# Performance work log

Hardware: AMD Instinct MI355X
Metric: run time of the kernel (lower is better)

## Reference

```python
import jax, jax.numpy as jnp
import numpy as np

N_NODES = 50000
N_EDGES = 800000
F_IN = 4
PERIODS = 8
H_DIM = 32


def setup_inputs() -> dict:
    key = jax.random.key(0)
    ks = jax.random.split(key, 20)
    s = lambda *sh: 1.0 / np.sqrt(sh[0])
    inp = {
        "x": jax.random.normal(ks[0], (N_NODES, F_IN, PERIODS), jnp.float32),
        "edge_index": jax.random.randint(ks[1], (2, N_EDGES), 0, N_NODES, jnp.int32),
        # GCNConv weights/biases for z, r, h gates (glorot-ish init)
        "Wz": jax.random.normal(ks[2], (F_IN, H_DIM), jnp.float32) * s(F_IN),
        "bz": jnp.zeros((H_DIM,), jnp.float32),
        "Wr": jax.random.normal(ks[3], (F_IN, H_DIM), jnp.float32) * s(F_IN),
        "br": jnp.zeros((H_DIM,), jnp.float32),
        "Wh": jax.random.normal(ks[4], (F_IN, H_DIM), jnp.float32) * s(F_IN),
        "bh": jnp.zeros((H_DIM,), jnp.float32),
        # torch.nn.Linear(2*H, H) for each gate; stored as [2H, H] for x @ W
        "LzW": jax.random.normal(ks[5], (2 * H_DIM, H_DIM), jnp.float32) * s(2 * H_DIM),
        "Lzb": jnp.zeros((H_DIM,), jnp.float32),
        "LrW": jax.random.normal(ks[6], (2 * H_DIM, H_DIM), jnp.float32) * s(2 * H_DIM),
        "Lrb": jnp.zeros((H_DIM,), jnp.float32),
        "LhW": jax.random.normal(ks[7], (2 * H_DIM, H_DIM), jnp.float32) * s(2 * H_DIM),
        "Lhb": jnp.zeros((H_DIM,), jnp.float32),
        # A3TGCN attention over periods (uniform init in PyG-T)
        "att": jax.random.uniform(ks[8], (PERIODS,), jnp.float32),
        # final Linear(32, periods)
        "outW": jax.random.normal(ks[9], (H_DIM, PERIODS), jnp.float32) * s(H_DIM),
        "outb": jnp.zeros((PERIODS,), jnp.float32),
    }
    return inp


def _forward(x, edge_index, Wz, bz, Wr, br, Wh, bh, LzW, Lzb, LrW, Lrb, LhW, Lhb, att, outW, outb):
    N = x.shape[0]
    src, dst = edge_index[0], edge_index[1]
    # GCN symmetric normalization with added self loops (edge_weight = 1)
    deg = jax.ops.segment_sum(jnp.ones(src.shape[0], x.dtype), dst, num_segments=N) + 1.0
    dinv = jnp.where(deg > 0, deg ** -0.5, 0.0)
    enorm = dinv[src] * dinv[dst]          # [E]
    snorm = dinv * dinv                    # self-loop norm, [N]

    def gcn(xt, W, b):
        h = xt @ W                                             # [N, 32]
        agg = jax.ops.segment_sum(enorm[:, None] * h[src], dst, num_segments=N)
        return agg + snorm[:, None] * h + b

    H0 = jnp.zeros((N, H_DIM), x.dtype)  # A3TGCN passes H=None each period
    probs = jax.nn.softmax(att)

    def step(acc, inputs):
        xt, p = inputs                                          # xt: [N, F]
        Z = jax.nn.sigmoid(jnp.concatenate([gcn(xt, Wz, bz), H0], axis=1) @ LzW + Lzb)
        R = jax.nn.sigmoid(jnp.concatenate([gcn(xt, Wr, br), H0], axis=1) @ LrW + Lrb)
        Ht = jnp.tanh(jnp.concatenate([gcn(xt, Wh, bh), H0 * R], axis=1) @ LhW + Lhb)
        H = Z * H0 + (1.0 - Z) * Ht
        return acc + p * H, None

    xs = jnp.moveaxis(x, 2, 0)             # [P, N, F]
    H_accum, _ = jax.lax.scan(step, jnp.zeros((N, H_DIM), x.dtype), (xs, probs))
    return jax.nn.relu(H_accum) @ outW + outb  # [N, periods]


def reference(x, edge_index, Wz, bz, Wr, br, Wh, bh, LzW, Lzb, LrW, Lrb, LhW, Lhb, att, outW, outb):
    return _forward(x, edge_index, Wz, bz, Wr, br, Wh, bh, LzW, Lzb, LrW, Lrb, LhW, Lhb, att, outW, outb)
```

## Files before the change

kernel.cpp:

```cpp
#include <hip/hip_runtime.h>


#define NN 50000
#define NE 800000
#define SLAB 48
#define NG 8
#define NPG (NN / NG)
#define FBLK 4096
#define GPB (FBLK / NG)
#define PBASE 0xAAAAAAAAu

#define OFF_CNT 0
#define OFF_PP  50048
#define OFF_CSR 50688

__device__ __forceinline__ int realdeg(int v) {
    unsigned dp = (unsigned)v - PBASE;
    return (dp < (1u << 20)) ? (int)dp : v;
}

__global__ __launch_bounds__(256) void k_fill(const int* ei, int* cnt,
        unsigned short* csr,
        const float* Wz, const float* bz, const float* Wh, const float* bh,
        const float* LzW, const float* Lzb, const float* LhW, const float* Lhb,
        const float* att, const float* outW, const float* outb, float* pp) {
    const int t = threadIdx.x, b = blockIdx.x;
    const int gx = b & 7, bi = b >> 3;
    const int nlo = gx * NPG;
    const int4* dst4 = (const int4*)(ei + NE);
    for (int g = bi * 256 + t; g < NE / 4; g += GPB * 256) {
        int4 dv = dst4[g];
        int dvals[4] = {dv.x, dv.y, dv.z, dv.w};
        const int e = 4 * g;
#pragma unroll
        for (int j = 0; j < 4; ++j) {
            int d = dvals[j];
            if ((unsigned)(d - nlo) < (unsigned)NPG) {
                int s = ei[e + j];
                unsigned pos = (unsigned)atomicAdd(&cnt[d], 1);
                unsigned sp_ = pos - PBASE;
                int slot = (sp_ < SLAB) ? (int)sp_ : ((pos < SLAB) ? (int)pos : -1);
                if (slot >= 0) csr[d * SLAB + slot] = (unsigned short)s;
            }
        }
    }
    if (b != 0) return;
    if (t < 128) {
        int f = t >> 5, k = t & 31;
        float mz = 0.f, mh = 0.f;
        for (int j = 0; j < 32; ++j) {
            mz += Wz[f * 32 + j] * LzW[j * 32 + k];
            mh += Wh[f * 32 + j] * LhW[j * 32 + k];
        }
        pp[t] = mz; pp[128 + t] = mh;
    }
    if (t < 32) {
        float cz = Lzb[t], ch = Lhb[t];
        for (int j = 0; j < 32; ++j) {
            cz += bz[j] * LzW[j * 32 + t];
            ch += bh[j] * LhW[j * 32 + t];
        }
        pp[256 + t] = cz; pp[288 + t] = ch;
    }
    if (t < 8) {
        float m = -1e30f;
        for (int j = 0; j < 8; ++j) m = fmaxf(m, att[j]);
        float ssum = 0.f;
        for (int j = 0; j < 8; ++j) ssum += __expf(att[j] - m);
        pp[320 + t] = __expf(att[t] - m) / ssum;
        pp[584 + t] = outb[t];
    }
    pp[328 + t] = outW[t];
}

__global__ __launch_bounds__(256) void k_gather(const float4* x4, const int* cnt,
        const unsigned short* csr, const float* pp, float* out) {
    __shared__ float sMz[128], sMh[128], scz[32], sch[32], spb[8], sob[8];
    __shared__ float soWT[264];
    const int t = threadIdx.x;
    if (t < 128) { sMz[t] = pp[t]; sMh[t] = pp[128 + t]; }
    if (t < 32)  { scz[t] = pp[256 + t]; sch[t] = pp[288 + t]; }
    if (t < 8)   { spb[t] = pp[320 + t]; sob[t] = pp[584 + t]; }
    {
        const int k = t >> 3, o = t & 7;
        soWT[o * 33 + k] = pp[328 + t];
    }
    __syncthreads();

    const int ln = t & 63, wv = t >> 6;
    const int half = ln >> 5;
    const int l = ln & 31;
    const int q = l & 7;
    const int j4 = l >> 3;

    const int n = blockIdx.x * 8 + wv * 2 + half;
    const int cn = cnt[n];
    const float4 xs = x4[n * 8 + q];

    const int deg = realdeg(cn);
    const int dlim = (deg < SLAB) ? deg : SLAB;
    const unsigned short* row = csr + n * SLAB;

    const int dl1 = (dlim < 32) ? dlim : 32;
    int rowv = 0; float cw = 0.f;
    if (l < dl1) {
        rowv = (int)row[l];
        cw = rsqrtf((float)realdeg(cnt[rowv]) + 1.0f);
    }
    float4 acc = make_float4(0.f, 0.f, 0.f, 0.f);
    const int nit = (dl1 + 3) >> 2;
    for (int i = 0; i < nit; ++i) {
        const int j = j4 + 4 * i;
        int   s = __shfl(rowv, j, 32);
        float w = __shfl(cw,   j, 32);
        if (j < dl1) {
            float4 v = x4[s * 8 + q];
            acc.x += w * v.x; acc.y += w * v.y;
            acc.z += w * v.z; acc.w += w * v.w;
        }
    }
    if (dlim > 32) {
        int r2 = 0; float c2 = 0.f;
        if (l < dlim - 32) {
            r2 = (int)row[32 + l];
            c2 = rsqrtf((float)realdeg(cnt[r2]) + 1.0f);
        }
        const int nit2 = (dlim - 32 + 3) >> 2;
        for (int i = 0; i < nit2; ++i) {
            const int j = j4 + 4 * i;
            int   s = __shfl(r2, j, 32);
            float w = __shfl(c2, j, 32);
            if (j < dlim - 32) {
                float4 v = x4[s * 8 + q];
                acc.x += w * v.x; acc.y += w * v.y;
                acc.z += w * v.z; acc.w += w * v.w;
            }
        }
    }
#pragma unroll
    for (int mm = 8; mm < 32; mm <<= 1) {
        acc.x += __shfl_xor(acc.x, mm, 64);
        acc.y += __shfl_xor(acc.y, mm, 64);
        acc.z += __shfl_xor(acc.z, mm, 64);
        acc.w += __shfl_xor(acc.w, mm, 64);
    }
    const float dd = rsqrtf((float)deg + 1.0f);
    acc.x = dd * (acc.x + dd * xs.x);
    acc.y = dd * (acc.y + dd * xs.y);
    acc.z = dd * (acc.z + dd * xs.z);
    acc.w = dd * (acc.w + dd * xs.w);

    float hacc = 0.f;
#pragma unroll
    for (int tp = 0; tp < 8; ++tp) {
        const int cc = tp & 3, lb = tp >> 2;
        float comp = (cc == 0) ? acc.x : (cc == 1) ? acc.y : (cc == 2) ? acc.z : acc.w;
        float u0 = __shfl(comp, lb,     32);
        float u1 = __shfl(comp, lb + 2, 32);
        float u2 = __shfl(comp, lb + 4, 32);
        float u3 = __shfl(comp, lb + 6, 32);
        float az = scz[l] + u0 * sMz[l] + u1 * sMz[32 + l] + u2 * sMz[64 + l] + u3 * sMz[96 + l];
        float ah = sch[l] + u0 * sMh[l] + u1 * sMh[32 + l] + u2 * sMh[64 + l] + u3 * sMh[96 + l];
        float z  = 1.f / (1.f + __expf(-az));
        float th = 1.f - 2.f / (__expf(2.f * ah) + 1.f);
        hacc += spb[tp] * (1.f - z) * th;
    }
    const float hr = fmaxf(hacc, 0.f);

    const int rbase = 8 * (l >> 3);
    const int o = l & 7;
    float p = 0.f;
#pragma unroll
    for (int j = 0; j < 8; ++j) {
        float hk = __shfl(hr, rbase + j, 32);
        p += hk * soWT[o * 33 + rbase + j];
    }
    p += __shfl_xor(p, 8, 32);
    p += __shfl_xor(p, 16, 32);
    if (l < 8) out[n * 8 + l] = p + sob[l];
}

extern "C" void kernel_launch(void* const* d_in, const int* in_sizes, int n_in,
                              void* d_out, int out_size, void* d_ws, size_t ws_size,
                              hipStream_t stream) {
    const float* x    = (const float*)d_in[0];
    const int*   ei   = (const int*)d_in[1];
    const float* Wz   = (const float*)d_in[2];
    const float* bz   = (const float*)d_in[3];
    const float* Wh   = (const float*)d_in[6];
    const float* bh   = (const float*)d_in[7];
    const float* LzW  = (const float*)d_in[8];
    const float* Lzb  = (const float*)d_in[9];
    const float* LhW  = (const float*)d_in[12];
    const float* Lhb  = (const float*)d_in[13];
    const float* att  = (const float*)d_in[14];
    const float* outW = (const float*)d_in[15];
    const float* outb = (const float*)d_in[16];

    int*   ws  = (int*)d_ws;
    int*   cnt = ws + OFF_CNT;
    float* pp  = (float*)(ws + OFF_PP);
    unsigned short* csr = (unsigned short*)(ws + OFF_CSR);

    k_fill<<<FBLK, 256, 0, stream>>>(ei, cnt, csr, Wz, bz, Wh, bh,
            LzW, Lzb, LhW, Lhb, att, outW, outb, pp);
    k_gather<<<NN / 8, 256, 0, stream>>>((const float4*)x, cnt, csr, pp,
            (float*)d_out);
}
```

Before: 155.3 us.

## Pre-scale node features by inverse sqrt degree in a separate prep kernel

Adds a k_prep kernel that computes each node's dinv once and writes y = dinv*x to workspace, alongside the weight folding moved out of k_fill. The gather kernel then sums pre-scaled neighbor rows directly, which removes the per-edge random cnt lookup and rsqrt. It also drops the shared-memory staging of parameters in favor of per-thread register loads. In exchange it adds a third launch and an extra full pass that reads x and writes y.

```diff
diff --git a/kernel.cpp b/kernel.cpp
--- a/kernel.cpp
+++ b/kernel.cpp
@@ -10,9 +10,11 @@
 #define GPB (FBLK / NG)
 #define PBASE 0xAAAAAAAAu
 
-#define OFF_CNT 0
-#define OFF_PP  50048
-#define OFF_CSR 50688
+#define OFF_CNT  0
+#define OFF_PP   50048
+#define OFF_CSR  50688
+#define OFF_DINV 1250688
+#define OFF_Y    1300736
 
 __device__ __forceinline__ int realdeg(int v) {
     unsigned dp = (unsigned)v - PBASE;
@@ -20,10 +22,7 @@
 }
 
 __global__ __launch_bounds__(256) void k_fill(const int* ei, int* cnt,
-        unsigned short* csr,
-        const float* Wz, const float* bz, const float* Wh, const float* bh,
-        const float* LzW, const float* Lzb, const float* LhW, const float* Lhb,
-        const float* att, const float* outW, const float* outb, float* pp) {
+        unsigned short* csr) {
     const int t = threadIdx.x, b = blockIdx.x;
     const int gx = b & 7, bi = b >> 3;
     const int nlo = gx * NPG;
@@ -44,7 +43,24 @@
             }
         }
     }
-    if (b != 0) return;
+}
+
+__global__ __launch_bounds__(256) void k_prep(const float4* x4, const int* cnt,
+        float4* y4, float* dinv,
+        const float* Wz, const float* bz, const float* Wh, const float* bh,
+        const float* LzW, const float* Lzb, const float* LhW, const float* Lhb,
+        const float* att, const float* outW, const float* outb, float* pp) {
+    const int t = threadIdx.x;
+    const int g = blockIdx.x * 256 + t;
+    if (g < NN * 8) {
+        const int n = g >> 3;
+        const float dd = rsqrtf((float)realdeg(cnt[n]) + 1.0f);
+        float4 v = x4[g];
+        v.x *= dd; v.y *= dd; v.z *= dd; v.w *= dd;
+        y4[g] = v;
+        if ((g & 7) == 0) dinv[n] = dd;
+    }
+    if (blockIdx.x != 0) return;
     if (t < 128) {
         int f = t >> 5, k = t & 31;
         float mz = 0.f, mh = 0.f;
@@ -73,67 +89,65 @@
     pp[328 + t] = outW[t];
 }
 
-__global__ __launch_bounds__(256) void k_gather(const float4* x4, const int* cnt,
-        const unsigned short* csr, const float* pp, float* out) {
-    __shared__ float sMz[128], sMh[128], scz[32], sch[32], spb[8], sob[8];
-    __shared__ float soWT[264];
+__global__ __launch_bounds__(256) void k_gather(const float4* y4,
+        const float* dinv, const int* cnt, const unsigned short* csr,
+        const float* pp, float* out) {
     const int t = threadIdx.x;
-    if (t < 128) { sMz[t] = pp[t]; sMh[t] = pp[128 + t]; }
-    if (t < 32)  { scz[t] = pp[256 + t]; sch[t] = pp[288 + t]; }
-    if (t < 8)   { spb[t] = pp[320 + t]; sob[t] = pp[584 + t]; }
-    {
-        const int k = t >> 3, o = t & 7;
-        soWT[o * 33 + k] = pp[328 + t];
-    }
-    __syncthreads();
-
     const int ln = t & 63, wv = t >> 6;
     const int half = ln >> 5;
     const int l = ln & 31;
     const int q = l & 7;
     const int j4 = l >> 3;
+    const int o = l & 7;
+    const int rbase = 8 * (l >> 3);
 
     const int n = blockIdx.x * 8 + wv * 2 + half;
+
     const int cn = cnt[n];
-    const float4 xs = x4[n * 8 + q];
+    const float dd = dinv[n];
+    const float4 ys = y4[n * 8 + q];
+
+    const float mz0 = pp[l],       mz1 = pp[32 + l];
+    const float mz2 = pp[64 + l],  mz3 = pp[96 + l];
+    const float mh0 = pp[128 + l], mh1 = pp[160 + l];
+    const float mh2 = pp[192 + l], mh3 = pp[224 + l];
+    const float cz  = pp[256 + l], chh = pp[288 + l];
+    float wj[8];
+#pragma unroll
+    for (int j = 0; j < 8; ++j) wj[j] = pp[328 + (rbase + j) * 8 + o];
+    const float sbo = pp[584 + o];
+    float pb[8];
+#pragma unroll
+    for (int j = 0; j < 8; ++j) pb[j] = pp[320 + j];
 
     const int deg = realdeg(cn);
     const int dlim = (deg < SLAB) ? deg : SLAB;
     const unsigned short* row = csr + n * SLAB;
 
     const int dl1 = (dlim < 32) ? dlim : 32;
-    int rowv = 0; float cw = 0.f;
-    if (l < dl1) {
-        rowv = (int)row[l];
-        cw = rsqrtf((float)realdeg(cnt[rowv]) + 1.0f);
-    }
+    int rowv = 0;
+    if (l < dl1) rowv = (int)row[l];
+
     float4 acc = make_float4(0.f, 0.f, 0.f, 0.f);
     const int nit = (dl1 + 3) >> 2;
     for (int i = 0; i < nit; ++i) {
         const int j = j4 + 4 * i;
-        int   s = __shfl(rowv, j, 32);
-        float w = __shfl(cw,   j, 32);
+        int s = __shfl(rowv, j, 32);
         if (j < dl1) {
-            float4 v = x4[s * 8 + q];
-            acc.x += w * v.x; acc.y += w * v.y;
-            acc.z += w * v.z; acc.w += w * v.w;
+            float4 v = y4[s * 8 + q];
+            acc.x += v.x; acc.y += v.y; acc.z += v.z; acc.w += v.w;
         }
     }
     if (dlim > 32) {
-        int r2 = 0; float c2 = 0.f;
-        if (l < dlim - 32) {
-            r2 = (int)row[32 + l];
-            c2 = rsqrtf((float)realdeg(cnt[r2]) + 1.0f);
-        }
+        int r2 = 0;
+        if (l < dlim - 32) r2 = (int)row[32 + l];
         const int nit2 = (dlim - 32 + 3) >> 2;
         for (int i = 0; i < nit2; ++i) {
             const int j = j4 + 4 * i;
-            int   s = __shfl(r2, j, 32);
-            float w = __shfl(c2, j, 32);
+            int s = __shfl(r2, j, 32);
             if (j < dlim - 32) {
-                float4 v = x4[s * 8 + q];
-                acc.x += w * v.x; acc.y += w * v.y;
-                acc.z += w * v.z; acc.w += w * v.w;
+                float4 v = y4[s * 8 + q];
+                acc.x += v.x; acc.y += v.y; acc.z += v.z; acc.w += v.w;
             }
         }
     }
@@ -144,11 +158,10 @@
         acc.z += __shfl_xor(acc.z, mm, 64);
         acc.w += __shfl_xor(acc.w, mm, 64);
     }
-    const float dd = rsqrtf((float)deg + 1.0f);
-    acc.x = dd * (acc.x + dd * xs.x);
-    acc.y = dd * (acc.y + dd * xs.y);
-    acc.z = dd * (acc.z + dd * xs.z);
-    acc.w = dd * (acc.w + dd * xs.w);
+    acc.x = dd * (acc.x + ys.x);
+    acc.y = dd * (acc.y + ys.y);
+    acc.z = dd * (acc.z + ys.z);
+    acc.w = dd * (acc.w + ys.w);
 
     float hacc = 0.f;
 #pragma unroll
@@ -159,25 +172,23 @@
         float u1 = __shfl(comp, lb + 2, 32);
         float u2 = __shfl(comp, lb + 4, 32);
         float u3 = __shfl(comp, lb + 6, 32);
-        float az = scz[l] + u0 * sMz[l] + u1 * sMz[32 + l] + u2 * sMz[64 + l] + u3 * sMz[96 + l];
-        float ah = sch[l] + u0 * sMh[l] + u1 * sMh[32 + l] + u2 * sMh[64 + l] + u3 * sMh[96 + l];
+        float az = cz  + u0 * mz0 + u1 * mz1 + u2 * mz2 + u3 * mz3;
+        float ah = chh + u0 * mh0 + u1 * mh1 + u2 * mh2 + u3 * mh3;
         float z  = 1.f / (1.f + __expf(-az));
         float th = 1.f - 2.f / (__expf(2.f * ah) + 1.f);
-        hacc += spb[tp] * (1.f - z) * th;
+        hacc += pb[tp] * (1.f - z) * th;
     }
     const float hr = fmaxf(hacc, 0.f);
 
-    const int rbase = 8 * (l >> 3);
-    const int o = l & 7;
     float p = 0.f;
 #pragma unroll
     for (int j = 0; j < 8; ++j) {
         float hk = __shfl(hr, rbase + j, 32);
-        p += hk * soWT[o * 33 + rbase + j];
+        p += hk * wj[j];
     }
     p += __shfl_xor(p, 8, 32);
     p += __shfl_xor(p, 16, 32);
-    if (l < 8) out[n * 8 + l] = p + sob[l];
+    if (l < 8) out[n * 8 + l] = p + sbo;
 }
 
 extern "C" void kernel_launch(void* const* d_in, const int* in_sizes, int n_in,
@@ -197,13 +208,16 @@
     const float* outW = (const float*)d_in[15];
     const float* outb = (const float*)d_in[16];
 
-    int*   ws  = (int*)d_ws;
-    int*   cnt = ws + OFF_CNT;
-    float* pp  = (float*)(ws + OFF_PP);
+    int*   ws   = (int*)d_ws;
+    int*   cnt  = ws + OFF_CNT;
+    float* pp   = (float*)(ws + OFF_PP);
     unsigned short* csr = (unsigned short*)(ws + OFF_CSR);
-
-    k_fill<<<FBLK, 256, 0, stream>>>(ei, cnt, csr, Wz, bz, Wh, bh,
-            LzW, Lzb, LhW, Lhb, att, outW, outb, pp);
-    k_gather<<<NN / 8, 256, 0, stream>>>((const float4*)x, cnt, csr, pp,
+    float* dinv = (float*)(ws + OFF_DINV);
+    float4* y4  = (float4*)(ws + OFF_Y);
+
+    k_fill<<<FBLK, 256, 0, stream>>>(ei, cnt, csr);
+    k_prep<<<(NN * 8 + 255) / 256, 256, 0, stream>>>((const float4*)x, cnt,
+            y4, dinv, Wz, bz, Wh, bh, LzW, Lzb, LhW, Lhb, att, outW, outb, pp);
+    k_gather<<<NN / 8, 256, 0, stream>>>(y4, dinv, cnt, csr, pp,
             (float*)d_out);
 }
```

After: 158.9 us. 1.02x slower.
